# Optimization experiments

Measured on AMD Instinct MI355X. Metric: run time of the kernel, lower is better.

The kernel has to match this reference:

```python
import jax, jax.numpy as jnp
import numpy as np

INP_SIZE = 1024
D_MODEL = 1024
B, S = 4, 2048


def setup_inputs() -> dict:
    key = jax.random.key(0)
    ks = jax.random.split(key, 9)
    q = jax.random.normal(ks[0], (B, S, INP_SIZE), dtype=jnp.float32)
    k = jax.random.normal(ks[1], (B, S, INP_SIZE), dtype=jnp.float32)
    v = jax.random.normal(ks[2], (B, S, INP_SIZE), dtype=jnp.float32)
    mask = jnp.zeros((1, S, S), dtype=jnp.float32)
    # learned params (random_normal init in keras)
    kernel_q = jax.random.normal(ks[3], (INP_SIZE, D_MODEL), dtype=jnp.float32) * 0.05
    kernel_k = jax.random.normal(ks[4], (INP_SIZE, D_MODEL), dtype=jnp.float32) * 0.05
    kernel_v = jax.random.normal(ks[5], (INP_SIZE, D_MODEL), dtype=jnp.float32) * 0.05
    bias_q = jax.random.normal(ks[6], (D_MODEL,), dtype=jnp.float32) * 0.05
    bias_k = jax.random.normal(ks[7], (D_MODEL,), dtype=jnp.float32) * 0.05
    bias_v = jax.random.normal(ks[8], (D_MODEL,), dtype=jnp.float32) * 0.05
    return {"q": q, "k": k, "v": v, "mask": mask,
            "kernel_q": kernel_q, "bias_q": bias_q,
            "kernel_k": kernel_k, "bias_k": bias_k,
            "kernel_v": kernel_v, "bias_v": bias_v}


def reference(q, k, v, mask, kernel_q, bias_q, kernel_k, bias_k, kernel_v, bias_v):
    # QKV projections (note: the original stores gelu activations but never
    # applies them in call(), so none are applied here).
    qp = jnp.einsum('bsi,id->bsd', q, kernel_q) + bias_q  # [B,S,D]
    kp = jnp.einsum('bsi,id->bsd', k, kernel_k) + bias_k
    vp = jnp.einsum('bsi,id->bsd', v, kernel_v) + bias_v
    dk = jnp.asarray(kp.shape[-1], dtype=jnp.float32)
    logits = jnp.einsum('bqd,bkd->bqk', qp, kp) / jnp.sqrt(dk)  # [B,S,S]
    logits = logits + mask  # additive mask, broadcasts over batch
    attn = jax.nn.softmax(logits, axis=-1)
    out = jnp.einsum('bqk,bkd->bqd', attn, vp)  # [B,S,D]
    return out
```

## Files before the change

### kernel.cpp

```cpp
#include <hip/hip_runtime.h>

typedef unsigned short u16;
typedef unsigned int u32;
typedef float f32x4 __attribute__((ext_vector_type(4)));
typedef __bf16 bf16x8 __attribute__((ext_vector_type(8)));

__device__ __forceinline__ u16 f2bf(float f) {
  u32 u = __float_as_uint(f);
  u += 0x7fffu + ((u >> 16) & 1u);
  return (u16)(u >> 16);
}
__device__ __forceinline__ float bf2f_lo(u32 w) { return __uint_as_float(w << 16); }
__device__ __forceinline__ float bf2f_hi(u32 w) { return __uint_as_float(w & 0xffff0000u); }

__device__ __forceinline__ void gload_lds16(const u16* g, u16* l) {
  __builtin_amdgcn_global_load_lds((const __attribute__((address_space(1))) void*)g,
                                   (__attribute__((address_space(3))) void*)l, 16, 0, 0);
}

__global__ __launch_bounds__(256)
void convert3_f32_bf16(const float* __restrict__ a, const float* __restrict__ b,
                       const float* __restrict__ c, u16* __restrict__ dst0, long n) {
  const float* src = blockIdx.z == 0 ? a : (blockIdx.z == 1 ? b : c);
  u16* dst = dst0 + (long)blockIdx.z * n;
  long stride = (long)gridDim.x * blockDim.x * 4;
  for (long i = ((long)blockIdx.x * blockDim.x + threadIdx.x) * 4; i < n; i += stride) {
    float4 v = *(const float4*)(src + i);
    ushort4 o;
    o.x = f2bf(v.x); o.y = f2bf(v.y); o.z = f2bf(v.z); o.w = f2bf(v.w);
    *(ushort4*)(dst + i) = o;
  }
}

__global__ __launch_bounds__(256)
void wtrans(const float* __restrict__ w0, const float* __restrict__ w1,
            const float* __restrict__ w2, u16* __restrict__ out0) {
  const float* src = blockIdx.z == 0 ? w0 : (blockIdx.z == 1 ? w1 : w2);
  u16* dst = out0 + (long)blockIdx.z * 1048576;
  __shared__ float tile[64][65];
  int t = threadIdx.x;
  int r = t >> 4, c4 = (t & 15) * 4;
  int kb = blockIdx.y * 64;
  int nb = blockIdx.x * 64;
#pragma unroll
  for (int rr = 0; rr < 64; rr += 16) {
    float4 v = *(const float4*)(src + (long)(kb + r + rr) * 1024 + nb + c4);
    tile[r + rr][c4 + 0] = v.x;
    tile[r + rr][c4 + 1] = v.y;
    tile[r + rr][c4 + 2] = v.z;
    tile[r + rr][c4 + 3] = v.w;
  }
  __syncthreads();
#pragma unroll
  for (int rr = 0; rr < 64; rr += 16) {
    ushort4 o;
    o.x = f2bf(tile[c4 + 0][r + rr]);
    o.y = f2bf(tile[c4 + 1][r + rr]);
    o.z = f2bf(tile[c4 + 2][r + rr]);
    o.w = f2bf(tile[c4 + 3][r + rr]);
    *(ushort4*)(dst + (long)(nb + r + rr) * 1024 + kb + c4) = o;
  }
}

template <int MODE>
__global__ __launch_bounds__(512, 2)
void gemm8(const u16* __restrict__ A, const u16* __restrict__ B,
           void* __restrict__ Cn, u16* __restrict__ Cct,
           const float* __restrict__ bqp, const float* __restrict__ bkp,
           const float* __restrict__ bvp,
           int M, int N, int K, long sA, long sB, long sC) {
  __shared__ u16 lds[2][2][16384];
  const int tid = threadIdx.x;
  const int wid = tid >> 6, lane = tid & 63;
  const int wr = wid >> 2, wc = wid & 3;
  const int l15 = lane & 15, l4 = lane >> 4;
  const int z = blockIdx.z;
  const u16* Ab = A + (long)z * sA;
  const u16* Bb = B + (long)z * sB;
  const int bm = blockIdx.x * 256;
  const int bnn = blockIdx.y * 256;

  f32x4 acc[8][4] = {};
  bf16x8 af[4][2], pb0[2][2], pb1[2][2];

#define STAGE_A(buf, mh, ks) {                                                \
    int d_ = ((mh) * 64 * 8) + tid;                                           \
    int r_ = d_ >> 3; int cs_ = (d_ & 7) ^ (r_ & 7);                          \
    gload_lds16(Ab + (long)(bm + r_) * K + (ks) + cs_ * 8,                    \
                &lds[buf][0][d_ * 8]);                                        \
    d_ += 1024; r_ = d_ >> 3; cs_ = (d_ & 7) ^ (r_ & 7);                      \
    gload_lds16(Ab + (long)(bm + r_) * K + (ks) + cs_ * 8,                    \
                &lds[buf][0][d_ * 8]);                                        \
  }

#define STAGE_B(buf, nh, ks)                                                  \
  _Pragma("unroll") for (int qq_ = 0; qq_ < 2; ++qq_) {                       \
    int u_ = qq_ * 512 + tid;                                                 \
    int s_ = u_ >> 8, w_ = u_ & 255;                                          \
    int r_ = s_ * 64 + (nh) * 32 + (w_ >> 3);                                 \
    int cs_ = (w_ & 7) ^ (r_ & 7);                                            \
    gload_lds16(Bb + (long)(bnn + r_) * K + (ks) + cs_ * 8,                   \
                &lds[buf][1][(r_ * 8 + (w_ & 7)) * 8]);                       \
  }

#define LDA(buf, mh)                                                          \
  _Pragma("unroll") for (int i_ = 0; i_ < 4; ++i_)                            \
  _Pragma("unroll") for (int kk_ = 0; kk_ < 2; ++kk_) {                       \
    int r_ = wr * 128 + (mh) * 64 + i_ * 16 + l15;                            \
    int cb_ = (kk_ * 4 + l4) ^ (r_ & 7);                                      \
    af[i_][kk_] = *(const bf16x8*)&lds[buf][0][(r_ * 8 + cb_) * 8];           \
  }

#define LDB(buf, nh, dst)                                                     \
  _Pragma("unroll") for (int j_ = 0; j_ < 2; ++j_)                            \
  _Pragma("unroll") for (int kk_ = 0; kk_ < 2; ++kk_) {                       \
    int r_ = wc * 64 + (nh) * 32 + j_ * 16 + l15;                             \
    int cb_ = (kk_ * 4 + l4) ^ (r_ & 7);                                      \
    dst[j_][kk_] = *(const bf16x8*)&lds[buf][1][(r_ * 8 + cb_) * 8];          \
  }

#define MF(mh, nh, bfr)                                                       \
  _Pragma("unroll") for (int kk_ = 0; kk_ < 2; ++kk_)                         \
  _Pragma("unroll") for (int i_ = 0; i_ < 4; ++i_)                            \
  _Pragma("unroll") for (int j_ = 0; j_ < 2; ++j_)                            \
    acc[(mh) * 4 + i_][(nh) * 2 + j_] = __builtin_amdgcn_mfma_f32_16x16x32_bf16( \
        af[i_][kk_], bfr[j_][kk_], acc[(mh) * 4 + i_][(nh) * 2 + j_], 0, 0, 0);

#define BAR __builtin_amdgcn_s_barrier()
#define LGKM0 asm volatile("s_waitcnt lgkmcnt(0)" ::: "memory")
#define LGKM8 asm volatile("s_waitcnt lgkmcnt(8)" ::: "memory")
#define VM6 asm volatile("s_waitcnt vmcnt(6)" ::: "memory")
#define PRIO1 __builtin_amdgcn_s_setprio(1)
#define PRIO0 __builtin_amdgcn_s_setprio(0)

  STAGE_A(0, 0, 0); STAGE_B(0, 0, 0); STAGE_B(0, 1, 0); STAGE_A(0, 1, 0);
  STAGE_A(1, 0, 64); STAGE_B(1, 0, 64); STAGE_B(1, 1, 64);
  VM6;
  BAR;

  for (int it = 0, nit = K >> 7; it < nit; ++it) {
    const int kt1 = it * 128 + 64;
    int ks0 = it * 128 + 128; if (ks0 >= K) ks0 -= K;
    int ks1 = kt1 + 128;      if (ks1 >= K) ks1 -= K;
    LDA(0, 0); LDB(0, 0, pb0); STAGE_A(1, 1, kt1);
    LGKM8; BAR; LGKM0;
    PRIO1; MF(0, 0, pb0); PRIO0; BAR;
    LDB(0, 1, pb1); STAGE_A(0, 0, ks0);
    BAR; LGKM0;
    PRIO1; MF(0, 1, pb1); PRIO0; BAR;
    LDA(0, 1); STAGE_B(0, 0, ks0);
    BAR; LGKM0;
    PRIO1; MF(1, 1, pb1); PRIO0; BAR;
    STAGE_B(0, 1, ks0); VM6;
    BAR;
    PRIO1; MF(1, 0, pb0); PRIO0; BAR;
    LDA(1, 0); LDB(1, 0, pb0); STAGE_A(0, 1, ks0);
    LGKM8; BAR; LGKM0;
    PRIO1; MF(0, 0, pb0); PRIO0; BAR;
    LDB(1, 1, pb1); STAGE_A(1, 0, ks1);
    BAR; LGKM0;
    PRIO1; MF(0, 1, pb1); PRIO0; BAR;
    LDA(1, 1); STAGE_B(1, 0, ks1);
    BAR; LGKM0;
    PRIO1; MF(1, 1, pb1); PRIO0; BAR;
    STAGE_B(1, 1, ks1); VM6;
    BAR;
    PRIO1; MF(1, 0, pb0); PRIO0; BAR;
  }
  asm volatile("s_waitcnt vmcnt(0)" ::: "memory");

  const int crow0 = bm + wr * 128 + l4 * 4;
  const int ccol0 = bnn + wc * 64 + l15;
  if constexpr (MODE == 0) {
    u16* Cp = (u16*)Cn + (long)z * sC;
#pragma unroll
    for (int m = 0; m < 8; ++m)
#pragma unroll
      for (int n = 0; n < 4; ++n)
#pragma unroll
        for (int r = 0; r < 4; ++r)
          Cp[(long)(crow0 + m * 16 + r) * N + (ccol0 + n * 16)] = f2bf(acc[m][n][r]);
  } else if constexpr (MODE == 1) {
    float* Cp = (float*)Cn + (long)z * sC;
#pragma unroll
    for (int m = 0; m < 8; ++m)
#pragma unroll
      for (int n = 0; n < 4; ++n)
#pragma unroll
        for (int r = 0; r < 4; ++r)
          Cp[(long)(crow0 + m * 16 + r) * N + (ccol0 + n * 16)] = acc[m][n][r];
  } else {
    const float* bias = z == 0 ? bqp : (z == 1 ? bkp : bvp);
    const float sc = z == 0 ? 0.03125f : 1.0f;
    if (z < 2) {
      u16* Cp = (u16*)Cn + (long)z * sC;
#pragma unroll
      for (int n = 0; n < 4; ++n) {
        float bb = bias[ccol0 + n * 16];
#pragma unroll
        for (int m = 0; m < 8; ++m)
#pragma unroll
          for (int r = 0; r < 4; ++r)
            Cp[(long)(crow0 + m * 16 + r) * N + (ccol0 + n * 16)] =
                f2bf((acc[m][n][r] + bb) * sc);
      }
    } else {
      const int batch = bm >> 11;
      u16* Cp = Cct + (long)batch * 2097152;
      const int sbase = (bm & 2047) + wr * 128 + l4 * 4;
#pragma unroll
      for (int n = 0; n < 4; ++n) {
        int d = ccol0 + n * 16;
        float bb = bias[d];
#pragma unroll
        for (int m = 0; m < 8; ++m) {
          ushort4 o;
          o.x = f2bf(acc[m][n][0] + bb);
          o.y = f2bf(acc[m][n][1] + bb);
          o.z = f2bf(acc[m][n][2] + bb);
          o.w = f2bf(acc[m][n][3] + bb);
          *(ushort4*)&Cp[(long)d * 2048 + sbase + m * 16] = o;
        }
      }
    }
  }
#undef STAGE_A
#undef STAGE_B
#undef LDA
#undef LDB
#undef MF
#undef BAR
#undef LGKM0
#undef LGKM8
#undef VM6
#undef PRIO1
#undef PRIO0
}

__device__ __forceinline__ float wave_max(float v) {
#pragma unroll
  for (int o = 32; o > 0; o >>= 1) v = fmaxf(v, __shfl_xor(v, o, 64));
  return v;
}
__device__ __forceinline__ float wave_sum(float v) {
#pragma unroll
  for (int o = 32; o > 0; o >>= 1) v += __shfl_xor(v, o, 64);
  return v;
}

__global__ __launch_bounds__(256)
void softmax_mask(u16* __restrict__ S, const float* __restrict__ mask) {
  long row = blockIdx.x;
  int q = (int)(row & 2047);
  u16* sp = S + row * 2048;
  const float* mp = mask + (long)q * 2048;
  int t = threadIdx.x;
  int wid = t >> 6;
  __shared__ float red[8];

  uint4 raw = *(const uint4*)(sp + t * 8);
  float4 m0 = *(const float4*)(mp + t * 8);
  float4 m1 = *(const float4*)(mp + t * 8 + 4);
  float x[8];
  x[0] = bf2f_lo(raw.x) + m0.x;
  x[1] = bf2f_hi(raw.x) + m0.y;
  x[2] = bf2f_lo(raw.y) + m0.z;
  x[3] = bf2f_hi(raw.y) + m0.w;
  x[4] = bf2f_lo(raw.z) + m1.x;
  x[5] = bf2f_hi(raw.z) + m1.y;
  x[6] = bf2f_lo(raw.w) + m1.z;
  x[7] = bf2f_hi(raw.w) + m1.w;

  float mx = x[0];
#pragma unroll
  for (int i = 1; i < 8; ++i) mx = fmaxf(mx, x[i]);
  mx = wave_max(mx);
  if ((t & 63) == 0) red[wid] = mx;
  __syncthreads();
  mx = fmaxf(fmaxf(red[0], red[1]), fmaxf(red[2], red[3]));

  float e[8], s = 0.f;
#pragma unroll
  for (int i = 0; i < 8; ++i) {
    e[i] = __expf(x[i] - mx);
    s += e[i];
  }
  s = wave_sum(s);
  if ((t & 63) == 0) red[4 + wid] = s;
  __syncthreads();
  s = (red[4] + red[5]) + (red[6] + red[7]);
  float inv = 1.f / s;

  uint4 outw;
  outw.x = (u32)f2bf(e[0] * inv) | ((u32)f2bf(e[1] * inv) << 16);
  outw.y = (u32)f2bf(e[2] * inv) | ((u32)f2bf(e[3] * inv) << 16);
  outw.z = (u32)f2bf(e[4] * inv) | ((u32)f2bf(e[5] * inv) << 16);
  outw.w = (u32)f2bf(e[6] * inv) | ((u32)f2bf(e[7] * inv) << 16);
  *(uint4*)(sp + t * 8) = outw;
}

extern "C" void kernel_launch(void* const* d_in, const int* in_sizes, int n_in,
                              void* d_out, int out_size, void* d_ws, size_t ws_size,
                              hipStream_t stream) {
  const float* q = (const float*)d_in[0];
  const float* k = (const float*)d_in[1];
  const float* v = (const float*)d_in[2];
  const float* mask = (const float*)d_in[3];
  const float* wq = (const float*)d_in[4];
  const float* bq = (const float*)d_in[5];
  const float* wk = (const float*)d_in[6];
  const float* bk = (const float*)d_in[7];
  const float* wv = (const float*)d_in[8];
  const float* bv = (const float*)d_in[9];
  float* out = (float*)d_out;

  u16* ws = (u16*)d_ws;
  const long NP = 8388608;
  u16* qp = ws;
  u16* kp = ws + NP;
  u16* vpT = ws + 2 * NP;
  u16* wT = ws + 3 * NP;
  u16* conv = ws + 3 * NP + 3145728;
  u16* S = conv;

  convert3_f32_bf16<<<dim3(2048, 1, 3), 256, 0, stream>>>(q, k, v, conv, NP);
  wtrans<<<dim3(16, 16, 3), 256, 0, stream>>>(wq, wk, wv, wT);
  gemm8<2><<<dim3(32, 4, 3), 512, 0, stream>>>(
      conv, wT, (void*)qp, vpT, bq, bk, bv, 8192, 1024, 1024, NP, 1048576, NP);
  gemm8<0><<<dim3(8, 8, 4), 512, 0, stream>>>(
      qp, kp, (void*)S, nullptr, nullptr, nullptr, nullptr,
      2048, 2048, 1024, 2097152, 2097152, 4194304);
  softmax_mask<<<dim3(8192, 1, 1), 256, 0, stream>>>(S, mask);
  gemm8<1><<<dim3(8, 4, 4), 512, 0, stream>>>(
      S, vpT, (void*)out, nullptr, nullptr, nullptr, nullptr,
      2048, 1024, 2048, 4194304, 2097152, 2097152);
}
```

Before: 354.0 us.

## Switch to fp16 MFMA and split-K the PV GEMM with a partial-sum add

Changes every intermediate and MFMA operand from bf16 to fp16. Splits the attention-times-V GEMM into two K halves across the z grid, doubling it from 128 to 256 blocks, and writes the second half into a float scratch buffer that a new addout kernel sums into the output. The split targets poor CU occupancy in the PV GEMM, and fp16 gives more mantissa precision. The cost is an extra kernel launch and an extra fp32 read-modify-write of the output, plus fp16 range risk on the logits.

After: 380.2 us. +7.4%, slower.

```diff
diff --git a/kernel.cpp b/kernel.cpp
--- a/kernel.cpp
+++ b/kernel.cpp
@@ -3,15 +3,17 @@
 typedef unsigned short u16;
 typedef unsigned int u32;
 typedef float f32x4 __attribute__((ext_vector_type(4)));
-typedef __bf16 bf16x8 __attribute__((ext_vector_type(8)));
-
-__device__ __forceinline__ u16 f2bf(float f) {
-  u32 u = __float_as_uint(f);
-  u += 0x7fffu + ((u >> 16) & 1u);
-  return (u16)(u >> 16);
-}
-__device__ __forceinline__ float bf2f_lo(u32 w) { return __uint_as_float(w << 16); }
-__device__ __forceinline__ float bf2f_hi(u32 w) { return __uint_as_float(w & 0xffff0000u); }
+typedef _Float16 h16x8 __attribute__((ext_vector_type(8)));
+
+__device__ __forceinline__ u16 f2h(float f) {
+  _Float16 h = (_Float16)f; u16 u; __builtin_memcpy(&u, &h, 2); return u;
+}
+__device__ __forceinline__ float h2f_lo(u32 w) {
+  u16 x = (u16)w; _Float16 h; __builtin_memcpy(&h, &x, 2); return (float)h;
+}
+__device__ __forceinline__ float h2f_hi(u32 w) {
+  u16 x = (u16)(w >> 16); _Float16 h; __builtin_memcpy(&h, &x, 2); return (float)h;
+}
 
 __device__ __forceinline__ void gload_lds16(const u16* g, u16* l) {
   __builtin_amdgcn_global_load_lds((const __attribute__((address_space(1))) void*)g,
@@ -19,15 +21,15 @@
 }
 
 __global__ __launch_bounds__(256)
-void convert3_f32_bf16(const float* __restrict__ a, const float* __restrict__ b,
-                       const float* __restrict__ c, u16* __restrict__ dst0, long n) {
+void convert3_f32_f16(const float* __restrict__ a, const float* __restrict__ b,
+                      const float* __restrict__ c, u16* __restrict__ dst0, long n) {
   const float* src = blockIdx.z == 0 ? a : (blockIdx.z == 1 ? b : c);
   u16* dst = dst0 + (long)blockIdx.z * n;
   long stride = (long)gridDim.x * blockDim.x * 4;
   for (long i = ((long)blockIdx.x * blockDim.x + threadIdx.x) * 4; i < n; i += stride) {
     float4 v = *(const float4*)(src + i);
     ushort4 o;
-    o.x = f2bf(v.x); o.y = f2bf(v.y); o.z = f2bf(v.z); o.w = f2bf(v.w);
+    o.x = f2h(v.x); o.y = f2h(v.y); o.z = f2h(v.z); o.w = f2h(v.w);
     *(ushort4*)(dst + i) = o;
   }
 }
@@ -54,10 +56,10 @@
 #pragma unroll
   for (int rr = 0; rr < 64; rr += 16) {
     ushort4 o;
-    o.x = f2bf(tile[c4 + 0][r + rr]);
-    o.y = f2bf(tile[c4 + 1][r + rr]);
-    o.z = f2bf(tile[c4 + 2][r + rr]);
-    o.w = f2bf(tile[c4 + 3][r + rr]);
+    o.x = f2h(tile[c4 + 0][r + rr]);
+    o.y = f2h(tile[c4 + 1][r + rr]);
+    o.z = f2h(tile[c4 + 2][r + rr]);
+    o.w = f2h(tile[c4 + 3][r + rr]);
     *(ushort4*)(dst + (long)(nb + r + rr) * 1024 + kb + c4) = o;
   }
 }
@@ -65,31 +67,33 @@
 template <int MODE>
 __global__ __launch_bounds__(512, 2)
 void gemm8(const u16* __restrict__ A, const u16* __restrict__ B,
-           void* __restrict__ Cn, u16* __restrict__ Cct,
+           void* __restrict__ Cn, void* __restrict__ Cct,
            const float* __restrict__ bqp, const float* __restrict__ bkp,
            const float* __restrict__ bvp,
-           int M, int N, int K, long sA, long sB, long sC) {
+           int M, int N, int K, int lda, int ldb, long sA, long sB, long sC) {
   __shared__ u16 lds[2][2][16384];
   const int tid = threadIdx.x;
   const int wid = tid >> 6, lane = tid & 63;
   const int wr = wid >> 2, wc = wid & 3;
   const int l15 = lane & 15, l4 = lane >> 4;
   const int z = blockIdx.z;
-  const u16* Ab = A + (long)z * sA;
-  const u16* Bb = B + (long)z * sB;
+  int zb = z, koff = 0;
+  if constexpr (MODE == 1) { zb = z >> 1; koff = (z & 1) * K; }
+  const u16* Ab = A + (long)zb * sA + koff;
+  const u16* Bb = B + (long)zb * sB + koff;
   const int bm = blockIdx.x * 256;
   const int bnn = blockIdx.y * 256;
 
   f32x4 acc[8][4] = {};
-  bf16x8 af[4][2], pb0[2][2], pb1[2][2];
+  h16x8 af[4][2], pb0[2][2], pb1[2][2];
 
 #define STAGE_A(buf, mh, ks) {                                                \
     int d_ = ((mh) * 64 * 8) + tid;                                           \
     int r_ = d_ >> 3; int cs_ = (d_ & 7) ^ (r_ & 7);                          \
-    gload_lds16(Ab + (long)(bm + r_) * K + (ks) + cs_ * 8,                    \
+    gload_lds16(Ab + (long)(bm + r_) * lda + (ks) + cs_ * 8,                  \
                 &lds[buf][0][d_ * 8]);                                        \
     d_ += 1024; r_ = d_ >> 3; cs_ = (d_ & 7) ^ (r_ & 7);                      \
-    gload_lds16(Ab + (long)(bm + r_) * K + (ks) + cs_ * 8,                    \
+    gload_lds16(Ab + (long)(bm + r_) * lda + (ks) + cs_ * 8,                  \
                 &lds[buf][0][d_ * 8]);                                        \
   }
 
@@ -99,7 +103,7 @@
     int s_ = u_ >> 8, w_ = u_ & 255;                                          \
     int r_ = s_ * 64 + (nh) * 32 + (w_ >> 3);                                 \
     int cs_ = (w_ & 7) ^ (r_ & 7);                                            \
-    gload_lds16(Bb + (long)(bnn + r_) * K + (ks) + cs_ * 8,                   \
+    gload_lds16(Bb + (long)(bnn + r_) * ldb + (ks) + cs_ * 8,                 \
                 &lds[buf][1][(r_ * 8 + (w_ & 7)) * 8]);                       \
   }
 
@@ -108,7 +112,7 @@
   _Pragma("unroll") for (int kk_ = 0; kk_ < 2; ++kk_) {                       \
     int r_ = wr * 128 + (mh) * 64 + i_ * 16 + l15;                            \
     int cb_ = (kk_ * 4 + l4) ^ (r_ & 7);                                      \
-    af[i_][kk_] = *(const bf16x8*)&lds[buf][0][(r_ * 8 + cb_) * 8];           \
+    af[i_][kk_] = *(const h16x8*)&lds[buf][0][(r_ * 8 + cb_) * 8];            \
   }
 
 #define LDB(buf, nh, dst)                                                     \
@@ -116,14 +120,14 @@
   _Pragma("unroll") for (int kk_ = 0; kk_ < 2; ++kk_) {                       \
     int r_ = wc * 64 + (nh) * 32 + j_ * 16 + l15;                             \
     int cb_ = (kk_ * 4 + l4) ^ (r_ & 7);                                      \
-    dst[j_][kk_] = *(const bf16x8*)&lds[buf][1][(r_ * 8 + cb_) * 8];          \
+    dst[j_][kk_] = *(const h16x8*)&lds[buf][1][(r_ * 8 + cb_) * 8];           \
   }
 
 #define MF(mh, nh, bfr)                                                       \
   _Pragma("unroll") for (int kk_ = 0; kk_ < 2; ++kk_)                         \
   _Pragma("unroll") for (int i_ = 0; i_ < 4; ++i_)                            \
   _Pragma("unroll") for (int j_ = 0; j_ < 2; ++j_)                            \
-    acc[(mh) * 4 + i_][(nh) * 2 + j_] = __builtin_amdgcn_mfma_f32_16x16x32_bf16( \
+    acc[(mh) * 4 + i_][(nh) * 2 + j_] = __builtin_amdgcn_mfma_f32_16x16x32_f16( \
         af[i_][kk_], bfr[j_][kk_], acc[(mh) * 4 + i_][(nh) * 2 + j_], 0, 0, 0);
 
 #define BAR __builtin_amdgcn_s_barrier()
@@ -172,16 +176,16 @@
   const int crow0 = bm + wr * 128 + l4 * 4;
   const int ccol0 = bnn + wc * 64 + l15;
   if constexpr (MODE == 0) {
-    u16* Cp = (u16*)Cn + (long)z * sC;
+    u16* Cp = (u16*)Cn + (long)zb * sC;
 #pragma unroll
     for (int m = 0; m < 8; ++m)
 #pragma unroll
       for (int n = 0; n < 4; ++n)
 #pragma unroll
         for (int r = 0; r < 4; ++r)
-          Cp[(long)(crow0 + m * 16 + r) * N + (ccol0 + n * 16)] = f2bf(acc[m][n][r]);
+          Cp[(long)(crow0 + m * 16 + r) * N + (ccol0 + n * 16)] = f2h(acc[m][n][r]);
   } else if constexpr (MODE == 1) {
-    float* Cp = (float*)Cn + (long)z * sC;
+    float* Cp = ((z & 1) == 0 ? (float*)Cn : (float*)Cct) + (long)zb * sC;
 #pragma unroll
     for (int m = 0; m < 8; ++m)
 #pragma unroll
@@ -202,11 +206,11 @@
 #pragma unroll
           for (int r = 0; r < 4; ++r)
             Cp[(long)(crow0 + m * 16 + r) * N + (ccol0 + n * 16)] =
-                f2bf((acc[m][n][r] + bb) * sc);
+                f2h((acc[m][n][r] + bb) * sc);
       }
     } else {
       const int batch = bm >> 11;
-      u16* Cp = Cct + (long)batch * 2097152;
+      u16* Cp = (u16*)Cct + (long)batch * 2097152;
       const int sbase = (bm & 2047) + wr * 128 + l4 * 4;
 #pragma unroll
       for (int n = 0; n < 4; ++n) {
@@ -215,10 +219,10 @@
 #pragma unroll
         for (int m = 0; m < 8; ++m) {
           ushort4 o;
-          o.x = f2bf(acc[m][n][0] + bb);
-          o.y = f2bf(acc[m][n][1] + bb);
-          o.z = f2bf(acc[m][n][2] + bb);
-          o.w = f2bf(acc[m][n][3] + bb);
+          o.x = f2h(acc[m][n][0] + bb);
+          o.y = f2h(acc[m][n][1] + bb);
+          o.z = f2h(acc[m][n][2] + bb);
+          o.w = f2h(acc[m][n][3] + bb);
           *(ushort4*)&Cp[(long)d * 2048 + sbase + m * 16] = o;
         }
       }
@@ -262,14 +266,14 @@
   float4 m0 = *(const float4*)(mp + t * 8);
   float4 m1 = *(const float4*)(mp + t * 8 + 4);
   float x[8];
-  x[0] = bf2f_lo(raw.x) + m0.x;
-  x[1] = bf2f_hi(raw.x) + m0.y;
-  x[2] = bf2f_lo(raw.y) + m0.z;
-  x[3] = bf2f_hi(raw.y) + m0.w;
-  x[4] = bf2f_lo(raw.z) + m1.x;
-  x[5] = bf2f_hi(raw.z) + m1.y;
-  x[6] = bf2f_lo(raw.w) + m1.z;
-  x[7] = bf2f_hi(raw.w) + m1.w;
+  x[0] = h2f_lo(raw.x) + m0.x;
+  x[1] = h2f_hi(raw.x) + m0.y;
+  x[2] = h2f_lo(raw.y) + m0.z;
+  x[3] = h2f_hi(raw.y) + m0.w;
+  x[4] = h2f_lo(raw.z) + m1.x;
+  x[5] = h2f_hi(raw.z) + m1.y;
+  x[6] = h2f_lo(raw.w) + m1.z;
+  x[7] = h2f_hi(raw.w) + m1.w;
 
   float mx = x[0];
 #pragma unroll
@@ -292,11 +296,22 @@
   float inv = 1.f / s;
 
   uint4 outw;
-  outw.x = (u32)f2bf(e[0] * inv) | ((u32)f2bf(e[1] * inv) << 16);
-  outw.y = (u32)f2bf(e[2] * inv) | ((u32)f2bf(e[3] * inv) << 16);
-  outw.z = (u32)f2bf(e[4] * inv) | ((u32)f2bf(e[5] * inv) << 16);
-  outw.w = (u32)f2bf(e[6] * inv) | ((u32)f2bf(e[7] * inv) << 16);
+  outw.x = (u32)f2h(e[0] * inv) | ((u32)f2h(e[1] * inv) << 16);
+  outw.y = (u32)f2h(e[2] * inv) | ((u32)f2h(e[3] * inv) << 16);
+  outw.z = (u32)f2h(e[4] * inv) | ((u32)f2h(e[5] * inv) << 16);
+  outw.w = (u32)f2h(e[6] * inv) | ((u32)f2h(e[7] * inv) << 16);
   *(uint4*)(sp + t * 8) = outw;
+}
+
+__global__ __launch_bounds__(256)
+void addout(float* __restrict__ out, const float* __restrict__ part, long n4) {
+  long stride = (long)gridDim.x * blockDim.x;
+  for (long i = (long)blockIdx.x * blockDim.x + threadIdx.x; i < n4; i += stride) {
+    float4 a = ((const float4*)out)[i];
+    float4 b = ((const float4*)part)[i];
+    a.x += b.x; a.y += b.y; a.z += b.z; a.w += b.w;
+    ((float4*)out)[i] = a;
+  }
 }
 
 extern "C" void kernel_launch(void* const* d_in, const int* in_sizes, int n_in,
@@ -322,16 +337,19 @@
   u16* wT = ws + 3 * NP;
   u16* conv = ws + 3 * NP + 3145728;
   u16* S = conv;
-
-  convert3_f32_bf16<<<dim3(2048, 1, 3), 256, 0, stream>>>(q, k, v, conv, NP);
+  float* pvpart = (float*)ws;
+
+  convert3_f32_f16<<<dim3(2048, 1, 3), 256, 0, stream>>>(q, k, v, conv, NP);
   wtrans<<<dim3(16, 16, 3), 256, 0, stream>>>(wq, wk, wv, wT);
   gemm8<2><<<dim3(32, 4, 3), 512, 0, stream>>>(
-      conv, wT, (void*)qp, vpT, bq, bk, bv, 8192, 1024, 1024, NP, 1048576, NP);
+      conv, wT, (void*)qp, (void*)vpT, bq, bk, bv,
+      8192, 1024, 1024, 1024, 1024, NP, 1048576, NP);
   gemm8<0><<<dim3(8, 8, 4), 512, 0, stream>>>(
       qp, kp, (void*)S, nullptr, nullptr, nullptr, nullptr,
-      2048, 2048, 1024, 2097152, 2097152, 4194304);
+      2048, 2048, 1024, 1024, 1024, 2097152, 2097152, 4194304);
   softmax_mask<<<dim3(8192, 1, 1), 256, 0, stream>>>(S, mask);
-  gemm8<1><<<dim3(8, 4, 4), 512, 0, stream>>>(
-      S, vpT, (void*)out, nullptr, nullptr, nullptr, nullptr,
-      2048, 1024, 2048, 4194304, 2097152, 2097152);
-}
+  gemm8<1><<<dim3(8, 4, 8), 512, 0, stream>>>(
+      S, vpT, (void*)out, (void*)pvpart, nullptr, nullptr, nullptr,
+      2048, 1024, 1024, 2048, 2048, 4194304, 2097152, 2097152);
+  addout<<<dim3(2048, 1, 1), 256, 0, stream>>>(out, pvpart, 2097152);
+}
```
